# Optimization experiments

Hardware: AMD Instinct MI355X
Metric: run time of the kernel (lower is better)

The kernel has to match this reference:

```python
import jax, jax.numpy as jnp
import numpy as np


def gatv2(x, src, dst, ea, Wl, bl, Wr, br, We, att, bias, N):
    # PyG GATv2Conv: source/target projections, edge embedding, leaky_relu(0.2)
    # attention, segment softmax over incoming edges, scatter-add aggregation.
    H, C = att.shape
    xl = (x @ Wl.T + bl).reshape(-1, H, C)   # [N,H,C] (source / message features)
    xr = (x @ Wr.T + br).reshape(-1, H, C)   # [N,H,C] (target features)
    ee = (ea @ We.T).reshape(-1, H, C)       # [E,H,C] edge embedding
    e = jax.nn.leaky_relu(xl[src] + xr[dst] + ee, 0.2)   # [E,H,C]
    s = jnp.einsum('ehc,hc->eh', e, att)                  # [E,H] scores
    smax = jax.ops.segment_max(s, dst, num_segments=N)
    ex = jnp.exp(s - smax[dst])
    den = jax.ops.segment_sum(ex, dst, num_segments=N)
    a = ex / (den[dst] + 1e-16)                           # segment softmax
    out = jax.ops.segment_sum(a[:, :, None] * xl[src], dst, num_segments=N)
    return out.reshape(N, H * C) + bias


def _forward(x, edge_index, edge_attr, actions, Wl1, bl1, Wr1, br1, We1, att1, bias1,
             Wl2, bl2, Wr2, br2, We2, att2, bias2, Wf, bf, Wp, bp, alpha):
    N = x.shape[0]
    E = edge_attr.shape[0]
    num_actions = E + 1
    src, dst = edge_index[0], edge_index[1]
    # add_self_loops(fill_value='mean'): self-loop edge_attr = per-node mean of incoming edge_attr
    cnt = jax.ops.segment_sum(jnp.ones((E,), x.dtype), dst, num_segments=N)
    mean_ea = jax.ops.segment_sum(edge_attr, dst, num_segments=N) / jnp.maximum(cnt, 1.0)[:, None]
    loop = jnp.arange(N, dtype=src.dtype)
    src2 = jnp.concatenate([src, loop])
    dst2 = jnp.concatenate([dst, loop])
    ea2 = jnp.concatenate([edge_attr, mean_ea], axis=0)
    h = jax.nn.relu(gatv2(x, src2, dst2, ea2, Wl1, bl1, Wr1, br1, We1, att1, bias1, N))
    h = jax.nn.relu(gatv2(h, src2, dst2, ea2, Wl2, bl2, Wr2, br2, We2, att2, bias2, N))
    g = jnp.mean(h, axis=0, keepdims=True)              # global_mean_pool, single graph -> [1,hid]
    state_potential = jax.nn.relu(g @ Wp.T + bp)[:, 0]  # [1]
    diag = jnp.concatenate([src != dst, jnp.array([True])])  # [E+1]
    logits = (g @ Wf.T + bf)[:, :num_actions]           # [1, E+1]
    amask = jnp.ones((num_actions,), bool).at[actions].set(False)
    mask = amask & diag
    logits = jnp.where(mask[None, :], logits, -jnp.inf)
    return jax.nn.softmax(logits, axis=1), state_potential, jax.nn.sigmoid(alpha)


def setup_inputs() -> dict:
    key = jax.random.key(0)
    ks = jax.random.split(key, 16)
    N, E, F, hid, H, A = 20000, 400000, 128, 64, 4, 450000
    x = jax.random.normal(ks[0], (N, F), jnp.float32)
    src = jax.random.randint(ks[1], (E,), 0, N)
    dst = (src + 1 + jax.random.randint(ks[2], (E,), 0, N - 1)) % N  # no pre-existing self loops
    edge_index = jnp.stack([src, dst])
    edge_attr = jax.random.normal(ks[3], (E, 1), jnp.float32)
    actions = jax.random.randint(ks[4], (128,), 0, E + 1)
    s = 0.05
    nrm = lambda k, shp: jax.random.normal(k, shp, jnp.float32) * s
    return {
        'x': x, 'edge_index': edge_index, 'edge_attr': edge_attr, 'actions': actions,
        'Wl1': nrm(ks[5], (H * hid, F)), 'bl1': jnp.zeros(H * hid),
        'Wr1': nrm(ks[6], (H * hid, F)), 'br1': jnp.zeros(H * hid),
        'We1': nrm(ks[7], (H * hid, 1)), 'att1': nrm(ks[8], (H, hid)), 'bias1': jnp.zeros(H * hid),
        'Wl2': nrm(ks[9], (hid, H * hid)), 'bl2': jnp.zeros(hid),
        'Wr2': nrm(ks[10], (hid, H * hid)), 'br2': jnp.zeros(hid),
        'We2': nrm(ks[11], (hid, 1)), 'att2': nrm(ks[12], (1, hid)), 'bias2': jnp.zeros(hid),
        'Wf': nrm(ks[13], (A, hid)), 'bf': jnp.zeros(A),
        'Wp': nrm(ks[14], (1, hid)), 'bp': jnp.zeros(1),
        'alpha': jnp.asarray(0.0, jnp.float32),
    }


def reference(x, edge_index, edge_attr, actions, Wl1, bl1, Wr1, br1, We1, att1, bias1,
              Wl2, bl2, Wr2, br2, We2, att2, bias2, Wf, bf, Wp, bp, alpha):
    return _forward(x, edge_index, edge_attr, actions, Wl1, bl1, Wr1, br1, We1, att1, bias1,
                    Wl2, bl2, Wr2, br2, We2, att2, bias2, Wf, bf, Wp, bp, alpha)
```

## Files before the change

kernel.cpp:

```cpp
#include <hip/hip_runtime.h>
#include <math.h>

typedef __attribute__((ext_vector_type(8))) short short8;
typedef __attribute__((ext_vector_type(4))) float f32x4;

__device__ __forceinline__ float wred_sum(float v) {
#pragma unroll
  for (int off = 32; off; off >>= 1) v += __shfl_xor(v, off, 64);
  return v;
}
__device__ __forceinline__ float wred_max(float v) {
#pragma unroll
  for (int off = 32; off; off >>= 1) v = fmaxf(v, __shfl_xor(v, off, 64));
  return v;
}
__device__ __forceinline__ unsigned f2key(float x) {
  unsigned b = __float_as_uint(x);
  return (b & 0x80000000u) ? ~b : (b | 0x80000000u);
}
__device__ __forceinline__ float key2f(unsigned k) {
  unsigned b = (k & 0x80000000u) ? (k & 0x7FFFFFFFu) : ~k;
  return __uint_as_float(b);
}
__device__ __forceinline__ float b2f(unsigned short u) {
  return __uint_as_float(((unsigned)u) << 16);
}
__device__ __forceinline__ unsigned short f2b(float f) {
  unsigned b = __float_as_uint(f);
  return (unsigned short)((b + 0x7FFFu + ((b >> 16) & 1u)) >> 16);
}

__global__ __launch_bounds__(256) void k_prep(
    const float* __restrict__ s0, ushort* __restrict__ d0, int n0,
    const float* __restrict__ s1, ushort* __restrict__ d1, int n1,
    const float* __restrict__ s2, ushort* __restrict__ d2, int n2,
    const float* __restrict__ s3, ushort* __restrict__ d3, int n3,
    const float* __restrict__ s4, ushort* __restrict__ d4, int n4,
    const int* __restrict__ dstv, const float* __restrict__ ea,
    int* __restrict__ cnt_i, float* __restrict__ sum_ea, int E,
    const int* __restrict__ actions, unsigned char* __restrict__ aflag,
    int n_act, int castB) {
  int b = blockIdx.x, tid = threadIdx.x;
  if (b == 0 && tid < n_act) aflag[actions[tid]] = 1;
  if (b < castB) {
    int t = (b * 256 + tid) * 4;
    const float* s; ushort* d; int off = t;
    if (off < n0) { s = s0; d = d0; }
    else { off -= n0;
      if (off < n1) { s = s1; d = d1; }
      else { off -= n1;
        if (off < n2) { s = s2; d = d2; }
        else { off -= n2;
          if (off < n3) { s = s3; d = d3; }
          else { off -= n3;
            if (off < n4) { s = s4; d = d4; }
            else return; } } } }
    float4 v = *(const float4*)(s + off);
    ushort4 o;
    o.x = f2b(v.x); o.y = f2b(v.y); o.z = f2b(v.z); o.w = f2b(v.w);
    *(ushort4*)(d + off) = o;
    return;
  }
  int e = (b - castB) * 256 + tid;
  if (e >= E) return;
  int d = dstv[e];
  atomicAdd(&cnt_i[d], 1);
  atomicAdd(&sum_ea[d], ea[e]);
}

__global__ __launch_bounds__(256) void k_gemm_scan(const ushort* __restrict__ A,
    const ushort* __restrict__ W0, const float* __restrict__ b0, ushort* __restrict__ C0,
    const ushort* __restrict__ W1, const float* __restrict__ b1, ushort* __restrict__ C1,
    int M, int Nc, int K,
    const int* __restrict__ cnt_i, int* __restrict__ row_st,
    int* __restrict__ cursor, int N) {
  int tid = threadIdx.x;
  if (blockIdx.z == 2) {
    if (blockIdx.x != 0 || blockIdx.y != 0) return;
    __shared__ int wtot[4];
    int per = (N + 255) / 256;
    int begin = tid * per, end = min(begin + per, N);
    int s = 0;
    for (int idx = begin; idx < end; ++idx) s += cnt_i[idx] + 1;
    int lane = tid & 63, w = tid >> 6;
    int inc = s;
#pragma unroll
    for (int off = 1; off < 64; off <<= 1) {
      int u = __shfl_up(inc, off, 64);
      if (lane >= off) inc += u;
    }
    if (lane == 63) wtot[w] = inc;
    __syncthreads();
    int woff = 0;
    for (int k = 0; k < w; ++k) woff += wtot[k];
    int run = woff + inc - s;
    for (int idx = begin; idx < end; ++idx) {
      row_st[idx] = run; cursor[idx] = run;
      run += cnt_i[idx] + 1;
    }
    if (tid == 255) row_st[N] = run;
    return;
  }
  const ushort* W = blockIdx.z ? W1 : W0;
  const float* bias = blockIdx.z ? b1 : b0;
  ushort* C = blockIdx.z ? C1 : C0;
  int wave = tid >> 6, lane = tid & 63;
  int m0 = blockIdx.x * 64 + wave * 16;
  int n0 = blockIdx.y * 64;
  int r = lane & 15, g = lane >> 4;
  f32x4 acc[4] = {};
  int am = min(m0 + r, M - 1);
  const ushort* Arow = A + (size_t)am * K + g * 8;
  const ushort* Wrow = W + (size_t)(n0 + r) * K + g * 8;
  for (int k0 = 0; k0 < K; k0 += 32) {
    short8 a = *(const short8*)(const void*)(Arow + k0);
#pragma unroll
    for (int c = 0; c < 4; ++c) {
      short8 b = *(const short8*)(const void*)(Wrow + (size_t)c * 16 * K + k0);
      acc[c] = __builtin_amdgcn_mfma_f32_16x16x32_bf16(a, b, acc[c], 0, 0, 0);
    }
  }
#pragma unroll
  for (int c = 0; c < 4; ++c) {
    int gn = n0 + c * 16 + r;
    float bv = bias[gn];
#pragma unroll
    for (int j = 0; j < 4; ++j) {
      int gm = m0 + g * 4 + j;
      if (gm < M) C[(size_t)gm * Nc + gn] = f2b(acc[c][j] + bv);
    }
  }
}

__global__ __launch_bounds__(256) void k_scatter(const int* __restrict__ dstv,
    const int* __restrict__ srcv, const float* __restrict__ ea,
    const int* __restrict__ cnt_i, const float* __restrict__ sum_ea,
    int* __restrict__ cursor, int* __restrict__ srcp, float* __restrict__ eap,
    int E, int E2) {
  int e = blockIdx.x * 256 + threadIdx.x;
  if (e >= E2) return;
  int d, sn; float av;
  if (e < E) { d = dstv[e]; sn = srcv[e]; av = ea[e]; }
  else { d = e - E; sn = d; av = sum_ea[d] / fmaxf((float)cnt_i[d], 1.0f); }
  int pos = atomicAdd(&cursor[d], 1);
  srcp[pos] = sn;
  eap[pos] = av;
}

__global__ __launch_bounds__(256) void k_gemm_mfma2(const ushort* __restrict__ A,
    const ushort* __restrict__ W0, const float* __restrict__ b0, ushort* __restrict__ C0,
    const ushort* __restrict__ W1, const float* __restrict__ b1, ushort* __restrict__ C1,
    int M, int Nc, int K) {
  const ushort* W = blockIdx.z ? W1 : W0;
  const float* bias = blockIdx.z ? b1 : b0;
  ushort* C = blockIdx.z ? C1 : C0;
  int wave = threadIdx.x >> 6, lane = threadIdx.x & 63;
  int m0 = blockIdx.x * 64 + wave * 16;
  int n0 = blockIdx.y * 64;
  int r = lane & 15, g = lane >> 4;
  f32x4 acc[4] = {};
  int am = min(m0 + r, M - 1);
  const ushort* Arow = A + (size_t)am * K + g * 8;
  const ushort* Wrow = W + (size_t)(n0 + r) * K + g * 8;
  for (int k0 = 0; k0 < K; k0 += 32) {
    short8 a = *(const short8*)(const void*)(Arow + k0);
#pragma unroll
    for (int c = 0; c < 4; ++c) {
      short8 b = *(const short8*)(const void*)(Wrow + (size_t)c * 16 * K + k0);
      acc[c] = __builtin_amdgcn_mfma_f32_16x16x32_bf16(a, b, acc[c], 0, 0, 0);
    }
  }
#pragma unroll
  for (int c = 0; c < 4; ++c) {
    int gn = n0 + c * 16 + r;
    float bv = bias[gn];
#pragma unroll
    for (int j = 0; j < 4; ++j) {
      int gm = m0 + g * 4 + j;
      if (gm < M) C[(size_t)gm * Nc + gn] = f2b(acc[c][j] + bv);
    }
  }
}

__global__ __launch_bounds__(256) void k_fused1(const ushort* __restrict__ xl,
    const ushort* __restrict__ xr, const int* __restrict__ srcp,
    const float* __restrict__ eap, const int* __restrict__ row_st,
    const float* __restrict__ We, const float* __restrict__ att,
    const float* __restrict__ bias, ushort* __restrict__ out, int N) {
  int tid = threadIdx.x;
  int lane = tid & 63;
  int half = lane >> 5, l32 = lane & 31;
  int n = blockIdx.x * 8 + (tid >> 6) * 2 + half;
  if (n >= N) return;
  int c0 = l32 * 8;
  float4 Wa = *(const float4*)(We + c0), Wb = *(const float4*)(We + c0 + 4);
  float4 Aa = *(const float4*)(att + c0), Ab = *(const float4*)(att + c0 + 4);
  float Wev[8] = {Wa.x, Wa.y, Wa.z, Wa.w, Wb.x, Wb.y, Wb.z, Wb.w};
  float atv[8] = {Aa.x, Aa.y, Aa.z, Aa.w, Ab.x, Ab.y, Ab.z, Ab.w};
  short8 xru = *(const short8*)(const void*)(xr + (size_t)n * 256 + c0);
  float xrf[8];
#pragma unroll
  for (int j = 0; j < 8; ++j) xrf[j] = b2f((unsigned short)xru[j]);
  int a = row_st[n], b = row_st[n + 1];
  float m = -INFINITY, den = 0.f;
  float acc[8] = {};
  int i = a;
  for (; i + 1 < b; i += 2) {
    int sn0 = srcp[i], sn1 = srcp[i + 1];
    float av0 = eap[i], av1 = eap[i + 1];
    short8 xu0 = *(const short8*)(const void*)(xl + (size_t)sn0 * 256 + c0);
    short8 xu1 = *(const short8*)(const void*)(xl + (size_t)sn1 * 256 + c0);
    float x0[8], x1[8];
    float t0 = 0.f, t1 = 0.f;
#pragma unroll
    for (int j = 0; j < 8; ++j) {
      x0[j] = b2f((unsigned short)xu0[j]);
      x1[j] = b2f((unsigned short)xu1[j]);
      float v0 = x0[j] + xrf[j] + av0 * Wev[j];
      float v1 = x1[j] + xrf[j] + av1 * Wev[j];
      v0 = v0 > 0.f ? v0 : 0.2f * v0;
      v1 = v1 > 0.f ? v1 : 0.2f * v1;
      t0 += atv[j] * v0;
      t1 += atv[j] * v1;
    }
    t0 += __shfl_xor(t0, 1, 8); t1 += __shfl_xor(t1, 1, 8);
    t0 += __shfl_xor(t0, 2, 8); t1 += __shfl_xor(t1, 2, 8);
    t0 += __shfl_xor(t0, 4, 8); t1 += __shfl_xor(t1, 4, 8);
    float tm = fmaxf(t0, t1);
    if (tm > m) {
      float sc = __expf(m - tm);
      m = tm; den *= sc;
#pragma unroll
      for (int j = 0; j < 8; ++j) acc[j] *= sc;
    }
    float e0 = __expf(t0 - m), e1 = __expf(t1 - m);
    den += e0 + e1;
#pragma unroll
    for (int j = 0; j < 8; ++j) acc[j] += e0 * x0[j] + e1 * x1[j];
  }
  if (i < b) {
    int sn = srcp[i];
    float av = eap[i];
    short8 xu = *(const short8*)(const void*)(xl + (size_t)sn * 256 + c0);
    float x[8];
    float t = 0.f;
#pragma unroll
    for (int j = 0; j < 8; ++j) {
      x[j] = b2f((unsigned short)xu[j]);
      float v = x[j] + xrf[j] + av * Wev[j];
      v = v > 0.f ? v : 0.2f * v;
      t += atv[j] * v;
    }
    t += __shfl_xor(t, 1, 8);
    t += __shfl_xor(t, 2, 8);
    t += __shfl_xor(t, 4, 8);
    if (t > m) {
      float sc = __expf(m - t);
      m = t; den *= sc;
#pragma unroll
      for (int j = 0; j < 8; ++j) acc[j] *= sc;
    }
    float ex = __expf(t - m);
    den += ex;
#pragma unroll
    for (int j = 0; j < 8; ++j) acc[j] += ex * x[j];
  }
  float inv = 1.f / (den + 1e-16f);
  float4 Ba = *(const float4*)(bias + c0), Bb = *(const float4*)(bias + c0 + 4);
  float bv[8] = {Ba.x, Ba.y, Ba.z, Ba.w, Bb.x, Bb.y, Bb.z, Bb.w};
  short8 o;
#pragma unroll
  for (int j = 0; j < 8; ++j) o[j] = (short)f2b(fmaxf(acc[j] * inv + bv[j], 0.f));
  *(short8*)(void*)(out + (size_t)n * 256 + c0) = o;
}

__global__ __launch_bounds__(256) void k_fused2(const ushort* __restrict__ xl,
    const ushort* __restrict__ xr, const int* __restrict__ srcp,
    const float* __restrict__ eap, const int* __restrict__ row_st,
    const float* __restrict__ We, const float* __restrict__ att,
    const float* __restrict__ bias, float* __restrict__ g_sum, int N) {
  __shared__ float gred[4][64];
  int tid = threadIdx.x;
  int lane = tid & 63, w = tid >> 6;
  int sub = lane >> 3, l8 = lane & 7;
  int n = blockIdx.x * 32 + w * 8 + sub;
  bool valid = n < N;
  int c0 = l8 * 8;
  float4 Wa = *(const float4*)(We + c0), Wb = *(const float4*)(We + c0 + 4);
  float4 Aa = *(const float4*)(att + c0), Ab = *(const float4*)(att + c0 + 4);
  float Wev[8] = {Wa.x, Wa.y, Wa.z, Wa.w, Wb.x, Wb.y, Wb.z, Wb.w};
  float atv[8] = {Aa.x, Aa.y, Aa.z, Aa.w, Ab.x, Ab.y, Ab.z, Ab.w};
  float xrf[8] = {};
  if (valid) {
    short8 xru = *(const short8*)(const void*)(xr + (size_t)n * 64 + c0);
#pragma unroll
    for (int j = 0; j < 8; ++j) xrf[j] = b2f((unsigned short)xru[j]);
  }
  int a = 0, b = 0;
  if (valid) { a = row_st[n]; b = row_st[n + 1]; }
  float m = -INFINITY, den = 0.f;
  float acc[8] = {};
  int i = a;
  for (; i + 1 < b; i += 2) {
    int sn0 = srcp[i], sn1 = srcp[i + 1];
    float av0 = eap[i], av1 = eap[i + 1];
    short8 xu0 = *(const short8*)(const void*)(xl + (size_t)sn0 * 64 + c0);
    short8 xu1 = *(const short8*)(const void*)(xl + (size_t)sn1 * 64 + c0);
    float x0[8], x1[8];
    float t0 = 0.f, t1 = 0.f;
#pragma unroll
    for (int j = 0; j < 8; ++j) {
      x0[j] = b2f((unsigned short)xu0[j]);
      x1[j] = b2f((unsigned short)xu1[j]);
      float v0 = x0[j] + xrf[j] + av0 * Wev[j];
      float v1 = x1[j] + xrf[j] + av1 * Wev[j];
      v0 = v0 > 0.f ? v0 : 0.2f * v0;
      v1 = v1 > 0.f ? v1 : 0.2f * v1;
      t0 += atv[j] * v0;
      t1 += atv[j] * v1;
    }
    t0 += __shfl_xor(t0, 1, 8); t1 += __shfl_xor(t1, 1, 8);
    t0 += __shfl_xor(t0, 2, 8); t1 += __shfl_xor(t1, 2, 8);
    t0 += __shfl_xor(t0, 4, 8); t1 += __shfl_xor(t1, 4, 8);
    float tm = fmaxf(t0, t1);
    if (tm > m) {
      float sc = __expf(m - tm);
      m = tm; den *= sc;
#pragma unroll
      for (int j = 0; j < 8; ++j) acc[j] *= sc;
    }
    float e0 = __expf(t0 - m), e1 = __expf(t1 - m);
    den += e0 + e1;
#pragma unroll
    for (int j = 0; j < 8; ++j) acc[j] += e0 * x0[j] + e1 * x1[j];
  }
  if (i < b) {
    int sn = srcp[i];
    float av = eap[i];
    short8 xu = *(const short8*)(const void*)(xl + (size_t)sn * 64 + c0);
    float x[8];
    float t = 0.f;
#pragma unroll
    for (int j = 0; j < 8; ++j) {
      x[j] = b2f((unsigned short)xu[j]);
      float v = x[j] + xrf[j] + av * Wev[j];
      v = v > 0.f ? v : 0.2f * v;
      t += atv[j] * v;
    }
    t += __shfl_xor(t, 1, 8);
    t += __shfl_xor(t, 2, 8);
    t += __shfl_xor(t, 4, 8);
    if (t > m) {
      float sc = __expf(m - t);
      m = t; den *= sc;
#pragma unroll
      for (int j = 0; j < 8; ++j) acc[j] *= sc;
    }
    float ex = __expf(t - m);
    den += ex;
#pragma unroll
    for (int j = 0; j < 8; ++j) acc[j] += ex * x[j];
  }
  float inv = 1.f / (den + 1e-16f);
  float4 Ba = *(const float4*)(bias + c0), Bb = *(const float4*)(bias + c0 + 4);
  float bv[8] = {Ba.x, Ba.y, Ba.z, Ba.w, Bb.x, Bb.y, Bb.z, Bb.w};
  float vals[8];
#pragma unroll
  for (int j = 0; j < 8; ++j)
    vals[j] = valid ? fmaxf(acc[j] * inv + bv[j], 0.f) : 0.f;
#pragma unroll
  for (int j = 0; j < 8; ++j) {
    float v = vals[j];
    v += __shfl_xor(v, 8, 64);
    v += __shfl_xor(v, 16, 64);
    v += __shfl_xor(v, 32, 64);
    vals[j] = v;
  }
  if (lane < 8) {
#pragma unroll
    for (int j = 0; j < 8; ++j) gred[w][lane * 8 + j] = vals[j];
  }
  __syncthreads();
  if (tid < 64)
    atomicAdd(&g_sum[tid], gred[0][tid] + gred[1][tid] + gred[2][tid] + gred[3][tid]);
}

__global__ __launch_bounds__(256) void k_logits(const float* __restrict__ g_sum,
    const float* __restrict__ Wp, const float* __restrict__ bp,
    const float* __restrict__ alpha,
    const float* __restrict__ Wf, const float* __restrict__ bf,
    const unsigned char* __restrict__ aflag, const int* __restrict__ src,
    const int* __restrict__ dst, float* __restrict__ logits,
    unsigned* __restrict__ gmax_key, float* __restrict__ out,
    int E, int NA, float invN) {
  __shared__ float gs[64];
  __shared__ float wmax[4];
  int tid = threadIdx.x;
  if (tid < 64) gs[tid] = g_sum[tid] * invN;
  __syncthreads();
  if (blockIdx.x == 0 && tid < 64) {
    float t = wred_sum(gs[tid] * Wp[tid]);
    if (tid == 0) {
      float sp = t + bp[0];
      out[NA] = sp > 0.f ? sp : 0.f;
      out[NA + 1] = 1.f / (1.f + __expf(-alpha[0]));
    }
  }
  int j0 = tid & 3;
  int row = blockIdx.x * 64 + (tid >> 2);
  float val = -INFINITY;
  if (row < NA) {
    const float4* wr = (const float4*)(Wf + (size_t)row * 64);
    const float4* g4 = (const float4*)gs;
    float acc = 0.f;
#pragma unroll
    for (int u = 0; u < 4; ++u) {
      float4 w = wr[j0 + u * 4];
      float4 gv = g4[j0 + u * 4];
      acc += w.x * gv.x + w.y * gv.y + w.z * gv.z + w.w * gv.w;
    }
    acc += __shfl_xor(acc, 1, 4);
    acc += __shfl_xor(acc, 2, 4);
    if (j0 == 0) {
      bool keep = (!aflag[row]) && (row >= E || src[row] != dst[row]);
      val = keep ? (acc + bf[row]) : -INFINITY;
      logits[row] = val;
    }
  }
  float mv = wred_max(val);
  if ((tid & 63) == 0) wmax[tid >> 6] = mv;
  __syncthreads();
  if (tid == 0) {
    float m = fmaxf(fmaxf(wmax[0], wmax[1]), fmaxf(wmax[2], wmax[3]));
    atomicMax(&gmax_key[blockIdx.x & 63], f2key(m));
  }
}

__global__ __launch_bounds__(256) void k_exp(float* __restrict__ logits,
    const unsigned* __restrict__ gmax_key, float* __restrict__ gsum, int NA) {
  __shared__ float wsum[4];
  int tid = threadIdx.x;
  float gmax = key2f(gmax_key[tid & 63]);
  gmax = wred_max(gmax);
  int i = (blockIdx.x * 256 + tid) * 4;
  float s = 0.f;
  if (i < NA) {
    float4 v = *(const float4*)(logits + i);
    float4 e;
    e.x = (i + 0 < NA && v.x != -INFINITY) ? __expf(v.x - gmax) : 0.f;
    e.y = (i + 1 < NA && v.y != -INFINITY) ? __expf(v.y - gmax) : 0.f;
    e.z = (i + 2 < NA && v.z != -INFINITY) ? __expf(v.z - gmax) : 0.f;
    e.w = (i + 3 < NA && v.w != -INFINITY) ? __expf(v.w - gmax) : 0.f;
    *(float4*)(logits + i) = e;
    s = e.x + e.y + e.z + e.w;
  }
  s = wred_sum(s);
  if ((tid & 63) == 0) wsum[tid >> 6] = s;
  __syncthreads();
  if (tid == 0)
    atomicAdd(gsum, wsum[0] + wsum[1] + wsum[2] + wsum[3]);
}

__global__ __launch_bounds__(256) void k_norm(const float* __restrict__ logits,
    const float* __restrict__ gsum, float* __restrict__ out, int NA) {
  int i = (blockIdx.x * 256 + threadIdx.x) * 4;
  if (i >= NA) return;
  float inv = 1.f / (*gsum);
  if (i + 3 < NA) {
    float4 v = *(const float4*)(logits + i);
    float4 o;
    o.x = v.x * inv; o.y = v.y * inv; o.z = v.z * inv; o.w = v.w * inv;
    *(float4*)(out + i) = o;
  } else {
    for (int j = i; j < NA; ++j) out[j] = logits[j] * inv;
  }
}

extern "C" void kernel_launch(void* const* d_in, const int* in_sizes, int n_in,
                              void* d_out, int out_size, void* d_ws, size_t ws_size,
                              hipStream_t stream) {
  const float* x      = (const float*)d_in[0];
  const int*   eidx   = (const int*)d_in[1];
  const float* eattr  = (const float*)d_in[2];
  const int*   actions= (const int*)d_in[3];
  const float* Wl1 = (const float*)d_in[4];
  const float* bl1 = (const float*)d_in[5];
  const float* Wr1 = (const float*)d_in[6];
  const float* br1 = (const float*)d_in[7];
  const float* We1 = (const float*)d_in[8];
  const float* att1= (const float*)d_in[9];
  const float* bias1=(const float*)d_in[10];
  const float* Wl2 = (const float*)d_in[11];
  const float* bl2 = (const float*)d_in[12];
  const float* Wr2 = (const float*)d_in[13];
  const float* br2 = (const float*)d_in[14];
  const float* We2 = (const float*)d_in[15];
  const float* att2= (const float*)d_in[16];
  const float* bias2=(const float*)d_in[17];
  const float* Wf  = (const float*)d_in[18];
  const float* bf  = (const float*)d_in[19];
  const float* Wp  = (const float*)d_in[20];
  const float* bp  = (const float*)d_in[21];
  const float* alpha=(const float*)d_in[22];

  const int F = 128;
  const int N = in_sizes[0] / F;
  const int E = in_sizes[2];
  const int E2 = E + N;
  const int NA = E + 1;
  const int n_act = in_sizes[3];
  const int* src = eidx;
  const int* dst = eidx + E;

  float* ws = (float*)d_ws;
  size_t p = 0;
  int*      cnt_i    = (int*)(ws + p);      p += (size_t)N;
  float*    sum_ea   = ws + p;              p += (size_t)N;
  float*    g_sum    = ws + p;              p += 64;
  unsigned* gmax_key = (unsigned*)(ws + p); p += 64;
  float*    gsum     = ws + p;              p += 64;
  unsigned char* aflag = (unsigned char*)(ws + p); p += ((size_t)NA + 3) / 4;
  size_t zero_bytes = p * sizeof(float);
  int*      row_st   = (int*)(ws + p);      p += (size_t)N + 64;
  int*      cursor   = (int*)(ws + p);      p += (size_t)N;
  int*      srcp     = (int*)(ws + p);      p += (size_t)E2;
  float*    eap      = ws + p;              p += (size_t)E2;
  float*    logits   = ws + p;              p += (size_t)NA + 64;
  p = (p + 3) & ~(size_t)3;
  ushort* ub = (ushort*)(ws + p);
  size_t q = 0;
  ushort* xb   = ub + q; q += (size_t)N * F;
  ushort* wl1b = ub + q; q += (size_t)256 * 128;
  ushort* wr1b = ub + q; q += (size_t)256 * 128;
  ushort* wl2b = ub + q; q += (size_t)64 * 256;
  ushort* wr2b = ub + q; q += (size_t)64 * 256;
  ushort* xl1b = ub + q; q += (size_t)N * 256;
  ushort* xr1b = ub + q; q += (size_t)N * 256;
  ushort* h1b  = ub + q; q += (size_t)N * 256;
  ushort* xl2b = ub + q; q += (size_t)N * 64;
  ushort* xr2b = ub + q; q += (size_t)N * 64;

  float* out = (float*)d_out;

  hipMemsetAsync(d_ws, 0, zero_bytes, stream);

  {
    int n0 = N * F, n1 = 256 * 128, n2 = 256 * 128, n3 = 64 * 256, n4 = 64 * 256;
    int tot4 = (n0 + n1 + n2 + n3 + n4) / 4;
    int castB = (tot4 + 255) / 256;
    int cntB = (E + 255) / 256;
    k_prep<<<castB + cntB, 256, 0, stream>>>(
        x, xb, n0, Wl1, wl1b, n1, Wr1, wr1b, n2, Wl2, wl2b, n3, Wr2, wr2b, n4,
        dst, eattr, cnt_i, sum_ea, E, actions, aflag, n_act, castB);
  }

  {
    dim3 g1((N + 63) / 64, 4, 3);
    k_gemm_scan<<<g1, 256, 0, stream>>>(xb, wl1b, bl1, xl1b, wr1b, br1, xr1b,
                                        N, 256, 128, cnt_i, row_st, cursor, N);
  }
  k_scatter<<<(E2 + 255) / 256, 256, 0, stream>>>(dst, src, eattr, cnt_i, sum_ea,
                                                  cursor, srcp, eap, E, E2);
  k_fused1<<<(N + 7) / 8, 256, 0, stream>>>(xl1b, xr1b, srcp, eap, row_st,
                                            We1, att1, bias1, h1b, N);
  {
    dim3 g2((N + 63) / 64, 1, 2);
    k_gemm_mfma2<<<g2, 256, 0, stream>>>(h1b, wl2b, bl2, xl2b, wr2b, br2, xr2b,
                                         N, 64, 256);
  }
  k_fused2<<<(N + 31) / 32, 256, 0, stream>>>(xl2b, xr2b, srcp, eap, row_st,
                                              We2, att2, bias2, g_sum, N);

  k_logits<<<(NA + 63) / 64, 256, 0, stream>>>(
      g_sum, Wp, bp, alpha, Wf, bf, aflag, src, dst,
      logits, gmax_key, out, E, NA, 1.0f / (float)N);
  int nb4 = (NA + 1023) / 1024;
  k_exp<<<nb4, 256, 0, stream>>>(logits, gmax_key, gsum, NA);
  k_norm<<<nb4, 256, 0, stream>>>(logits, gsum, out, NA);
}
```

Before: 294.3 us.

## Split CSR scan into wide single-block kernel and fuse edge scatter into GEMM launch

The prefix scan over per-node counts moves from one 256-thread block that walks sequential chunks into its own 1024-thread block-wide scan kernel. The edge scatter into CSR order now runs as an extra z-slice of the first-layer GEMM grid, using a grid-stride loop. This overlaps the scatter with the projection GEMM and removes one launch, but adds a separate small scan launch. Only the GEMM's z-slice blocks do the scatter, so its parallelism is limited to the GEMM grid's x*y size.

```diff
diff --git a/kernel.cpp b/kernel.cpp
--- a/kernel.cpp
+++ b/kernel.cpp
@@ -68,37 +68,64 @@
   atomicAdd(&sum_ea[d], ea[e]);
 }
 
-__global__ __launch_bounds__(256) void k_gemm_scan(const ushort* __restrict__ A,
+__global__ __launch_bounds__(1024) void k_scan(const int* __restrict__ cnt_i,
+    int* __restrict__ row_st, int* __restrict__ cursor, int N) {
+  __shared__ int ws[16];
+  int tid = threadIdx.x;
+  int lane = tid & 63, w = tid >> 6;
+  int running = 0;
+  for (int base = 0; base < N; base += 1024) {
+    int i = base + tid;
+    int c = (i < N) ? (cnt_i[i] + 1) : 0;
+    int inc = c;
+#pragma unroll
+    for (int off = 1; off < 64; off <<= 1) {
+      int u = __shfl_up(inc, off, 64);
+      if (lane >= off) inc += u;
+    }
+    if (lane == 63) ws[w] = inc;
+    __syncthreads();
+    if (tid < 16) {
+      int s = ws[tid];
+#pragma unroll
+      for (int off = 1; off < 16; off <<= 1) {
+        int u = __shfl_up(s, off, 16);
+        if (tid >= off) s += u;
+      }
+      ws[tid] = s;
+    }
+    __syncthreads();
+    int woff = (w == 0) ? 0 : ws[w - 1];
+    int total = ws[15];
+    int ex = running + woff + (inc - c);
+    if (i < N) { row_st[i] = ex; cursor[i] = ex; }
+    running += total;
+    __syncthreads();
+  }
+  if (tid == 0) row_st[N] = running;
+}
+
+__global__ __launch_bounds__(256) void k_gemm_scatter(const ushort* __restrict__ A,
     const ushort* __restrict__ W0, const float* __restrict__ b0, ushort* __restrict__ C0,
     const ushort* __restrict__ W1, const float* __restrict__ b1, ushort* __restrict__ C1,
     int M, int Nc, int K,
-    const int* __restrict__ cnt_i, int* __restrict__ row_st,
-    int* __restrict__ cursor, int N) {
+    const int* __restrict__ dstv, const int* __restrict__ srcv,
+    const float* __restrict__ ea, const int* __restrict__ cnt_i,
+    const float* __restrict__ sum_ea,
+    int* __restrict__ cursor, int* __restrict__ srcp, float* __restrict__ eap,
+    int E, int E2) {
   int tid = threadIdx.x;
   if (blockIdx.z == 2) {
-    if (blockIdx.x != 0 || blockIdx.y != 0) return;
-    __shared__ int wtot[4];
-    int per = (N + 255) / 256;
-    int begin = tid * per, end = min(begin + per, N);
-    int s = 0;
-    for (int idx = begin; idx < end; ++idx) s += cnt_i[idx] + 1;
-    int lane = tid & 63, w = tid >> 6;
-    int inc = s;
-#pragma unroll
-    for (int off = 1; off < 64; off <<= 1) {
-      int u = __shfl_up(inc, off, 64);
-      if (lane >= off) inc += u;
-    }
-    if (lane == 63) wtot[w] = inc;
-    __syncthreads();
-    int woff = 0;
-    for (int k = 0; k < w; ++k) woff += wtot[k];
-    int run = woff + inc - s;
-    for (int idx = begin; idx < end; ++idx) {
-      row_st[idx] = run; cursor[idx] = run;
-      run += cnt_i[idx] + 1;
-    }
-    if (tid == 255) row_st[N] = run;
+    int flat = blockIdx.x * gridDim.y + blockIdx.y;
+    int stride = gridDim.x * gridDim.y * 256;
+    for (int e = flat * 256 + tid; e < E2; e += stride) {
+      int d, sn; float av;
+      if (e < E) { d = dstv[e]; sn = srcv[e]; av = ea[e]; }
+      else { d = e - E; sn = d; av = sum_ea[d] / fmaxf((float)cnt_i[d], 1.0f); }
+      int pos = atomicAdd(&cursor[d], 1);
+      srcp[pos] = sn;
+      eap[pos] = av;
+    }
     return;
   }
   const ushort* W = blockIdx.z ? W1 : W0;
@@ -130,21 +157,6 @@
       if (gm < M) C[(size_t)gm * Nc + gn] = f2b(acc[c][j] + bv);
     }
   }
-}
-
-__global__ __launch_bounds__(256) void k_scatter(const int* __restrict__ dstv,
-    const int* __restrict__ srcv, const float* __restrict__ ea,
-    const int* __restrict__ cnt_i, const float* __restrict__ sum_ea,
-    int* __restrict__ cursor, int* __restrict__ srcp, float* __restrict__ eap,
-    int E, int E2) {
-  int e = blockIdx.x * 256 + threadIdx.x;
-  if (e >= E2) return;
-  int d, sn; float av;
-  if (e < E) { d = dstv[e]; sn = srcv[e]; av = ea[e]; }
-  else { d = e - E; sn = d; av = sum_ea[d] / fmaxf((float)cnt_i[d], 1.0f); }
-  int pos = atomicAdd(&cursor[d], 1);
-  srcp[pos] = sn;
-  eap[pos] = av;
 }
 
 __global__ __launch_bounds__(256) void k_gemm_mfma2(const ushort* __restrict__ A,
@@ -554,13 +566,15 @@
         dst, eattr, cnt_i, sum_ea, E, actions, aflag, n_act, castB);
   }
 
+  k_scan<<<1, 1024, 0, stream>>>(cnt_i, row_st, cursor, N);
+
   {
     dim3 g1((N + 63) / 64, 4, 3);
-    k_gemm_scan<<<g1, 256, 0, stream>>>(xb, wl1b, bl1, xl1b, wr1b, br1, xr1b,
-                                        N, 256, 128, cnt_i, row_st, cursor, N);
-  }
-  k_scatter<<<(E2 + 255) / 256, 256, 0, stream>>>(dst, src, eattr, cnt_i, sum_ea,
-                                                  cursor, srcp, eap, E, E2);
+    k_gemm_scatter<<<g1, 256, 0, stream>>>(xb, wl1b, bl1, xl1b, wr1b, br1, xr1b,
+                                           N, 256, 128,
+                                           dst, src, eattr, cnt_i, sum_ea,
+                                           cursor, srcp, eap, E, E2);
+  }
   k_fused1<<<(N + 7) / 8, 256, 0, stream>>>(xl1b, xr1b, srcp, eap, row_st,
                                             We1, att1, bias1, h1b, N);
   {
```

After: 273.1 us. -7.2%, faster.
